# Kernel tuning notes

Measured on AMD Instinct MI355X. Metric: run time of the kernel, lower is better.

The kernel has to match this reference:

```python
import jax, jax.numpy as jnp
import numpy as np

N, L, LEADS = 512, 640, 3
COND_DIM, NUM_K, DIM_K = 1, 100, 5
FLAT = 256 * 79  # 20224, from conv stack trace


def _leaky(x):
    return jnp.where(x >= 0, x, 0.2 * x)


def _sn(w, u):
    # PyTorch spectral_norm: one power iteration (u, v detached), sigma = u^T W v
    wm = w.reshape(w.shape[0], -1)
    v = wm.T @ u
    v = v / (jnp.linalg.norm(v) + 1e-12)
    u2 = wm @ v
    u2 = u2 / (jnp.linalg.norm(u2) + 1e-12)
    u2 = jax.lax.stop_gradient(u2)
    v = jax.lax.stop_gradient(v)
    sigma = u2 @ (wm @ v)
    return w / sigma


def _conv1d(x, w, b, stride, pad):
    y = jax.lax.conv_general_dilated(
        x, w, window_strides=(stride,), padding=[(pad, pad)],
        dimension_numbers=('NCH', 'OIH', 'NCH'))
    return y + b[None, :, None]


def setup_inputs() -> dict:
    key = jax.random.key(0)
    ks = jax.random.split(key, 16)
    g = lambda k, shp, s: (jax.random.normal(k, shp, dtype=jnp.float32) * s)
    inp = {
        'ecg': jax.random.normal(ks[0], (N, L, LEADS), dtype=jnp.float32),
        'condition': jax.random.randint(ks[1], (N, 1), 0, 4),
        'w1': g(ks[2], (64, LEADS, 5), 0.2), 'b1': jnp.zeros((64,), jnp.float32),
        'u1': jax.random.normal(ks[3], (64,), dtype=jnp.float32),
        'w2': g(ks[4], (128, 64, 7), 0.05), 'b2': jnp.zeros((128,), jnp.float32),
        'u2': jax.random.normal(ks[5], (128,), dtype=jnp.float32),
        'w3': g(ks[6], (256, 128, 9), 0.03), 'b3': jnp.zeros((256,), jnp.float32),
        'u3': jax.random.normal(ks[7], (256,), dtype=jnp.float32),
        'emb': g(ks[8], (4, COND_DIM), 1.0),
        'cond_w': g(ks[9], (50, COND_DIM), 0.5), 'cond_b': jnp.zeros((50,), jnp.float32),
        'mb_w': g(ks[10], (FLAT, NUM_K * DIM_K), 0.01),
        'fc_w': g(ks[11], (1, FLAT + NUM_K + 50), 0.01), 'fc_b': jnp.zeros((1,), jnp.float32),
    }
    return inp


def reference(ecg, condition, w1, b1, u1, w2, b2, u2, w3, b3, u3,
              emb, cond_w, cond_b, mb_w, fc_w, fc_b):
    # condition embedding -> Linear(cond_dim, 50)
    cemb = emb[condition[:, 0]]                       # [N, cond_dim]
    cond = cemb @ cond_w.T + cond_b                   # [N, 50]

    x = ecg.transpose(0, 2, 1)                        # [N, 3, 640]
    x = _leaky(_conv1d(x, _sn(w1, u1), b1, 2, 4))     # [N, 64, 322]
    x = _leaky(_conv1d(x, _sn(w2, u2), b2, 2, 3))     # [N, 128, 161]
    x = _leaky(_conv1d(x, _sn(w3, u3), b3, 2, 2))     # [N, 256, 79]
    flat = x.reshape(x.shape[0], -1)                  # [N, 20224]

    # minibatch discrimination
    act = (flat @ mb_w).reshape(-1, NUM_K, DIM_K)     # [N, K, D]
    l1 = jnp.abs(act[:, None] - act[None, :]).sum(-1)  # [N, N, K]
    feats = jnp.exp(-l1).sum(axis=1)                  # [N, K]

    out = jnp.concatenate([flat, feats, cond], axis=1)
    return out @ fc_w.T + fc_b                        # [N, 1]
```

## Files before the change

kernel.cpp:

```cpp
#include <hip/hip_runtime.h>
#include <math.h>

#define NB 512
#define LIN 640
#define NLEADS 3
#define L1O 322
#define L2O 161
#define L3O 79
#define C1N 64
#define C2N 128
#define C3N 256
#define FLATSZ 20224
#define NUMK 100
#define DIMK 5
#define SPLITK 8

typedef __attribute__((ext_vector_type(8))) short short8;
typedef __attribute__((ext_vector_type(4))) float f32x4;

__device__ __forceinline__ unsigned short f2bf(float x){
  unsigned u = __builtin_bit_cast(unsigned, x);
  unsigned r = u + 0x7FFFu + ((u >> 16) & 1u);
  return (unsigned short)(r >> 16);
}
__device__ __forceinline__ float bf2f(unsigned short x){
  unsigned u = ((unsigned)x) << 16;
  return __builtin_bit_cast(float, u);
}

__device__ __forceinline__ float block_reduce_sum(float val, float* red){
#pragma unroll
  for(int off=32; off>0; off>>=1) val += __shfl_down(val, off, 64);
  int lane = threadIdx.x & 63;
  int wv = threadIdx.x >> 6;
  if(lane==0) red[wv] = val;
  __syncthreads();
  int nw = blockDim.x >> 6;
  float r = red[0];
  for(int i=1;i<nw;i++) r += red[i];
  __syncthreads();
  return r;
}

__global__ __launch_bounds__(256)
void sn_pass1(const float* __restrict__ w1, const float* __restrict__ u1,
              const float* __restrict__ w2, const float* __restrict__ u2,
              const float* __restrict__ w3, const float* __restrict__ u3,
              float* __restrict__ v_all, float* __restrict__ ss){
  __shared__ float red[4];
  int b = blockIdx.x, tid = threadIdx.x;
  const float* w; const float* u; int O, C, off, c, widx;
  if(b==0){ w=w1; u=u1; O=64;  C=15;   off=0;   c=tid;            widx=0; }
  else if(b<3){ w=w2; u=u2; O=128; C=448; off=16;  c=(b-1)*256+tid; widx=1; }
  else { w=w3; u=u3; O=256; C=1152; off=464; c=(b-3)*256+tid;      widx=2; }
  float vv = 0.f;
  if(c < C){
    for(int o=0;o<O;o+=4){
      vv += w[(o+0)*C+c]*u[o+0] + w[(o+1)*C+c]*u[o+1]
          + w[(o+2)*C+c]*u[o+2] + w[(o+3)*C+c]*u[o+3];
    }
    v_all[off + c] = vv;
  }
  float ps = (c < C) ? vv*vv : 0.f;
  float tot = block_reduce_sum(ps, red);
  if(tid==0) atomicAdd(&ss[widx], tot);
}

__global__ __launch_bounds__(256)
void sn_pass2(const float* __restrict__ w1, const float* __restrict__ w2,
              const float* __restrict__ w3, const float* __restrict__ v_all,
              float* __restrict__ Sun){
  int b = blockIdx.x, tid = threadIdx.x;
  int lane = tid & 63, wv = tid >> 6;
  const float* w; int C, off, o, widx;
  if(b < 16){ w=w1; C=15;   off=0;   o=b*4+wv;      widx=0; }
  else if(b < 48){ w=w2; C=448; off=16;  o=(b-16)*4+wv; widx=1; }
  else { w=w3; C=1152; off=464; o=(b-48)*4+wv;          widx=2; }
  float t = 0.f;
  for(int c=lane; c<C; c+=64) t += w[o*C+c]*v_all[off+c];
#pragma unroll
  for(int s=32; s>0; s>>=1) t += __shfl_down(t, s, 64);
  if(lane==0) atomicAdd(&Sun[widx], t*t);
}

__global__ void wprep_kernel(const float* __restrict__ w1, const float* __restrict__ w2,
                             const float* __restrict__ w3, const float* __restrict__ ss,
                             const float* __restrict__ Sun,
                             unsigned short* __restrict__ w1p, unsigned short* __restrict__ w2p,
                             unsigned short* __restrict__ w3p){
  float sc[3];
#pragma unroll
  for(int i=0;i<3;i++){
    float inv = 1.f/(sqrtf(ss[i])+1e-12f);
    float S = Sun[i]*inv*inv;
    sc[i] = (sqrtf(S)+1e-12f)/S;
  }
  int idx = blockIdx.x*256 + threadIdx.x;
  if(idx < C1N*32){
    int o = idx >> 5, kk = idx & 31;
    w1p[idx] = (kk < 15) ? f2bf(w1[o*15+kk]*sc[0]) : 0;
  }
  if(idx < C2N*448){
    int o = idx / 448, k2 = idx - o*448;
    int r = k2 >> 6, i = k2 & 63;
    w2p[idx] = f2bf(w2[o*448 + i*7 + r]*sc[1]);
  }
  if(idx < C3N*1152){
    int o = idx / 1152, k2 = idx - o*1152;
    int r = k2 >> 7, i = k2 & 127;
    w3p[idx] = f2bf(w3[o*1152 + i*9 + r]*sc[2]);
  }
}

__global__ __launch_bounds__(256, 2)
void conv123_mfma(const float* __restrict__ ecg, const unsigned short* __restrict__ w1p,
                  const float* __restrict__ b1, const unsigned short* __restrict__ w2p,
                  const float* __restrict__ b2, const unsigned short* __restrict__ w3p,
                  const float* __restrict__ b3, unsigned short* __restrict__ flatbf){
  __shared__ unsigned short y2buf[22712];
  __shared__ unsigned short slabs[13600];
  __shared__ unsigned short B1s[3328];
  int n = blockIdx.x, tid = threadIdx.x;
  int lane = tid & 63, w = tid >> 6;

  if(tid < 136){
    y2buf[tid] = 0;
    y2buf[82*136 + tid] = 0;
    y2buf[83*136 + tid] = 0;
    y2buf[11424 + tid] = 0;
    y2buf[11424 + 81*136 + tid] = 0;
    y2buf[11424 + 82*136 + tid] = 0;
  }

  const float* eb = ecg + (size_t)n*LIN*NLEADS;
  f32x4 zero4 = {0.f,0.f,0.f,0.f};

  for(int tile=0; tile<2; tile++){
    int c0    = tile ? 189 : 0;
    int tbase = tile ? 96  : 0;
    int suboff= tile ? -94 : 2;

    __syncthreads();
    {
      uint4 z = {0u,0u,0u,0u};
      uint4* zd = (uint4*)slabs;
#pragma unroll
      for(int q=0;q<7;q++){
        int f = q*256 + tid;
        if(f < 1700) zd[f] = z;
      }
    }
    if(tid < 208){
      int t1 = c0 + tid;
      int p0 = 2*t1 - 4;
      unsigned short row16[16];
      row16[15] = 0;
      if(p0 >= 0 && p0 <= 635){
        const float* f = eb + p0*NLEADS;
#pragma unroll
        for(int rp=0; rp<5; rp++)
#pragma unroll
          for(int i=0;i<3;i++)
            row16[i*5+rp] = f2bf(f[3*rp+i]);
      } else {
#pragma unroll
        for(int rp=0; rp<5; rp++){
          int p = p0 + rp;
          bool ok = (unsigned)p < (unsigned)LIN;
#pragma unroll
          for(int i=0;i<3;i++)
            row16[i*5+rp] = ok ? f2bf(eb[p*NLEADS+i]) : (unsigned short)0;
        }
      }
      unsigned* dst = (unsigned*)(B1s + tid*16);
#pragma unroll
      for(int q=0;q<8;q++)
        dst[q] = (unsigned)row16[2*q] | ((unsigned)row16[2*q+1] << 16);
    }
    __syncthreads();

    {
      short8 a1 = *(const short8*)(w1p + ((w*16 + (lane&15))<<5) + (lane>>4)*8);
      int cfrag = lane >> 4;
#pragma unroll
      for(int half=0; half<2; half++){
        int nt0 = half*7, ntc = half ? 6 : 7;
        f32x4 c1[7];
        for(int j=0;j<ntc;j++){
          int tp = (nt0+j)*16 + (lane&15);
          short8 b = {0,0,0,0,0,0,0,0};
          if(cfrag < 2) b = *(const short8*)(B1s + tp*16 + cfrag*8);
          c1[j] = __builtin_amdgcn_mfma_f32_16x16x32_bf16(a1, b, zero4, 0, 0, 0);
        }
#pragma unroll
        for(int reg=0;reg<4;reg++){
          int o = w*16 + (lane>>4)*4 + reg;
          float bias = b1[o];
          for(int j=0;j<ntc;j++){
            int tp = (nt0+j)*16 + (lane&15);
            int t1 = c0 + tp;
            int sub = (t1>>1) + suboff;
            if(t1 < L1O && sub < 100){
              float v = c1[j][reg] + bias;
              v = v>=0.f ? v : 0.2f*v;
              slabs[((t1&1)?6800:0) + sub*68 + o] = f2bf(v);
            }
          }
        }
      }
    }
    __syncthreads();

    f32x4 acc[2][6];
#pragma unroll
    for(int i=0;i<2;i++)
#pragma unroll
      for(int j=0;j<6;j++) acc[i][j] = zero4;

    const unsigned short* w2base = w2p + ((size_t)(w*2*16 + (lane&15)))*448 + (lane>>4)*8;
    short8 a_cur[2];
    a_cur[0] = *(const short8*)(w2base);
    a_cur[1] = *(const short8*)(w2base + 16*448);

    for(int ck=0; ck<14; ck++){
      short8 a_nxt[2];
      if(ck < 13){
        a_nxt[0] = *(const short8*)(w2base + (ck+1)*32);
        a_nxt[1] = *(const short8*)(w2base + 16*448 + (ck+1)*32);
      }
      int r = ck >> 1, i0 = (ck & 1)*32;
      int p = (r+1) & 1;
      int m = ((r-3) - p) >> 1;
      int base = (p?6800:0) + (m+2 + (lane&15))*68 + i0 + (lane>>4)*8;
      short8 b[6];
#pragma unroll
      for(int nt=0;nt<6;nt++)
        b[nt] = *(const short8*)(slabs + base + nt*16*68);
      __builtin_amdgcn_s_setprio(1);
#pragma unroll
      for(int mm=0;mm<2;mm++)
#pragma unroll
        for(int nt=0;nt<6;nt++)
          acc[mm][nt] = __builtin_amdgcn_mfma_f32_16x16x32_bf16(a_cur[mm], b[nt], acc[mm][nt], 0, 0, 0);
      __builtin_amdgcn_s_setprio(0);
      if(ck < 13){ a_cur[0] = a_nxt[0]; a_cur[1] = a_nxt[1]; }
    }

#pragma unroll
    for(int mm=0;mm<2;mm++){
#pragma unroll
      for(int reg=0;reg<4;reg++){
        int o = (w*2+mm)*16 + (lane>>4)*4 + reg;
        float bias = b2[o];
#pragma unroll
        for(int nt=0;nt<6;nt++){
          int tl = nt*16 + (lane&15);
          int t = tbase + tl;
          if(t < L2O){
            float v = acc[mm][nt][reg] + bias;
            v = v>=0.f ? v : 0.2f*v;
            y2buf[((t&1)?11424:0) + ((t>>1)+1)*136 + o] = f2bf(v);
          }
        }
      }
    }
  }
  __syncthreads();

  f32x4 acc3[4][5];
#pragma unroll
  for(int i=0;i<4;i++)
#pragma unroll
    for(int j=0;j<5;j++) acc3[i][j] = zero4;

  const unsigned short* wbase = w3p + ((size_t)(w*64) + (lane&15))*1152 + (lane>>4)*8;
  short8 abuf[3][4];
#pragma unroll
  for(int d=0; d<2; d++)
#pragma unroll
    for(int mm=0;mm<4;mm++)
      abuf[d][mm] = *(const short8*)(wbase + mm*16*1152 + d*32);

#pragma unroll
  for(int ck=0; ck<36; ck++){
    const int cur = ck % 3;
    const int nxt = (ck+2) % 3;
    if(ck+2 < 36){
      int kc = (ck+2)*32;
#pragma unroll
      for(int mm=0;mm<4;mm++)
        abuf[nxt][mm] = *(const short8*)(wbase + mm*16*1152 + kc);
    }
    int r = ck >> 2, i0 = (ck & 3) * 32;
    int cbase = ((r & 1) ? 11424 : 0) + (r >> 1)*136 + i0 + (lane>>4)*8;
    short8 b[5];
#pragma unroll
    for(int nt=0;nt<5;nt++){
      int t = nt*16 + (lane&15);
      b[nt] = *(const short8*)(y2buf + cbase + t*136);
    }
    __builtin_amdgcn_s_setprio(1);
#pragma unroll
    for(int mm=0;mm<4;mm++)
#pragma unroll
      for(int nt=0;nt<5;nt++)
        acc3[mm][nt] = __builtin_amdgcn_mfma_f32_16x16x32_bf16(abuf[cur][mm], b[nt], acc3[mm][nt], 0, 0, 0);
    __builtin_amdgcn_s_setprio(0);
  }
#pragma unroll
  for(int mm=0;mm<4;mm++){
#pragma unroll
    for(int reg=0;reg<4;reg++){
      int o = w*64 + mm*16 + (lane>>4)*4 + reg;
      float bias = b3[o];
#pragma unroll
      for(int nt=0;nt<5;nt++){
        int t = nt*16 + (lane&15);
        if(t < L3O){
          float v = acc3[mm][nt][reg] + bias;
          v = v>=0.f ? v : 0.2f*v;
          flatbf[(size_t)n*FLATSZ + o*L3O + t] = f2bf(v);
        }
      }
    }
  }
}

__global__ __launch_bounds__(256)
void mbw_transpose(const float* __restrict__ mbw, unsigned short* __restrict__ mbwT){
  __shared__ unsigned short tile[32][36];
  int k0 = blockIdx.x*32, n0 = blockIdx.y*32, tid = threadIdx.x;
  int r = tid >> 3, c4 = (tid & 7) * 4;
  int nbase = n0 + c4;
  if(nbase + 3 < 500){
    float4 v = *(const float4*)(mbw + (size_t)(k0+r)*500 + nbase);
    tile[r][c4+0] = f2bf(v.x);
    tile[r][c4+1] = f2bf(v.y);
    tile[r][c4+2] = f2bf(v.z);
    tile[r][c4+3] = f2bf(v.w);
  } else {
#pragma unroll
    for(int j=0;j<4;j++){
      int nn = nbase + j;
      float v = (nn < 500) ? mbw[(size_t)(k0+r)*500 + nn] : 0.f;
      tile[r][c4+j] = f2bf(v);
    }
  }
  __syncthreads();
  int nl = tid >> 3, kq = (tid & 7) * 4;
  unsigned short t0 = tile[kq+0][nl], t1 = tile[kq+1][nl];
  unsigned short t2 = tile[kq+2][nl], t3 = tile[kq+3][nl];
  uint2 p;
  p.x = (unsigned)t0 | ((unsigned)t1 << 16);
  p.y = (unsigned)t2 | ((unsigned)t3 << 16);
  *(uint2*)(mbwT + (size_t)(n0+nl)*FLATSZ + k0 + kq) = p;
}

__global__ __launch_bounds__(256)
void mb_gemm_mfma(const unsigned short* __restrict__ flatbf, const unsigned short* __restrict__ mbwT,
                  float* __restrict__ part){
  __shared__ unsigned short As[64*32];
  __shared__ unsigned short Bs[64*32];
  int tid = threadIdx.x;
  int lane = tid & 63, w = tid >> 6;
  int m0 = blockIdx.x*64, n0 = blockIdx.y*64, bz = blockIdx.z;
  int t_count = 79;
  int k0 = bz*79*32;
  f32x4 zero = {0.f,0.f,0.f,0.f};
  f32x4 acc[4];
#pragma unroll
  for(int i=0;i<4;i++) acc[i] = zero;
  int arow = tid >> 2, acol = (tid & 3) * 8;
  for(int t=0; t<t_count; t++, k0+=32){
    __syncthreads();
    ((uint4*)As)[tid] = *(const uint4*)(flatbf + (size_t)(m0+arow)*FLATSZ + k0 + acol);
    ((uint4*)Bs)[tid] = *(const uint4*)(mbwT  + (size_t)(n0+arow)*FLATSZ + k0 + acol);
    __syncthreads();
    short8 a = *(const short8*)(As + (w*16 + (lane&15))*32 + (lane>>4)*8);
#pragma unroll
    for(int nt=0;nt<4;nt++){
      short8 b = *(const short8*)(Bs + (nt*16 + (lane&15))*32 + (lane>>4)*8);
      acc[nt] = __builtin_amdgcn_mfma_f32_16x16x32_bf16(a, b, acc[nt], 0, 0, 0);
    }
  }
  float* po = part + (size_t)bz*NB*500;
#pragma unroll
  for(int nt=0;nt<4;nt++){
#pragma unroll
    for(int reg=0;reg<4;reg++){
      int m = m0 + w*16 + (lane>>4)*4 + reg;
      int c = n0 + nt*16 + (lane&15);
      if(c < 500) po[(size_t)m*500 + c] = acc[nt][reg];
    }
  }
}

__global__ void mb_reduce_kernel(const float* __restrict__ part, float* __restrict__ actT){
  int idx = blockIdx.x*256 + threadIdx.x;
  float s = 0.f;
#pragma unroll
  for(int z=0;z<SPLITK;z++) s += part[(size_t)z*NB*500 + idx];
  int n = idx/500, c = idx - n*500;
  actT[(size_t)c*NB + n] = s;
}

__global__ __launch_bounds__(256)
void feats_kernel(const float* __restrict__ actT, float* __restrict__ feats){
  __shared__ float ash[4][50];
  __shared__ float pred[4][4];
  int i0 = blockIdx.x*4, k0 = blockIdx.y*10;
  int tid = threadIdx.x, lane = tid & 63, wv = tid >> 6;
  if(tid < 200){
    int ii = tid/50, c = tid - ii*50;
    ash[ii][c] = actT[(size_t)(k0*5+c)*NB + i0 + ii];
  }
  __syncthreads();
  const float LOG2E = 1.4426950408889634f;
  int j1 = tid, j2 = tid + 256;
  for(int kk=0; kk<10; kk++){
    const float* r0 = actT + (size_t)(k0+kk)*5*NB;
    float xa0=r0[j1], xa1=r0[NB+j1], xa2=r0[2*NB+j1], xa3=r0[3*NB+j1], xa4=r0[4*NB+j1];
    float xb0=r0[j2], xb1=r0[NB+j2], xb2=r0[2*NB+j2], xb3=r0[3*NB+j2], xb4=r0[4*NB+j2];
    float f[4];
#pragma unroll
    for(int ii=0; ii<4; ii++){
      float a0=ash[ii][kk*5+0], a1=ash[ii][kk*5+1], a2=ash[ii][kk*5+2],
            a3=ash[ii][kk*5+3], a4=ash[ii][kk*5+4];
      float la = fabsf(xa0-a0)+fabsf(xa1-a1)+fabsf(xa2-a2)+fabsf(xa3-a3)+fabsf(xa4-a4);
      float lb = fabsf(xb0-a0)+fabsf(xb1-a1)+fabsf(xb2-a2)+fabsf(xb3-a3)+fabsf(xb4-a4);
      f[ii] = exp2f(-LOG2E*la) + exp2f(-LOG2E*lb);
    }
#pragma unroll
    for(int ii=0; ii<4; ii++){
      float v = f[ii];
#pragma unroll
      for(int s=32; s>0; s>>=1) v += __shfl_down(v, s, 64);
      if(lane==0) pred[wv][ii] = v;
    }
    __syncthreads();
    if(tid < 4){
      float v = pred[0][tid] + pred[1][tid] + pred[2][tid] + pred[3][tid];
      feats[(size_t)(i0+tid)*NUMK + k0 + kk] = v;
    }
    __syncthreads();
  }
}

__global__ void final_kernel(const unsigned short* __restrict__ flatbf, const float* __restrict__ feats,
                             const int* __restrict__ condition, const float* __restrict__ emb,
                             const float* __restrict__ cond_w, const float* __restrict__ cond_b,
                             const float* __restrict__ fc_w, const float* __restrict__ fc_b,
                             float* __restrict__ out){
  __shared__ float red[4];
  int n = blockIdx.x, tid = threadIdx.x;
  float s = 0.f;
  const unsigned short* fr = flatbf + (size_t)n*FLATSZ;
  for(int q=tid; q<FLATSZ/8; q+=256){
    uint4 u = *(const uint4*)(fr + q*8);
    float4 wa = *(const float4*)(fc_w + q*8);
    float4 wb = *(const float4*)(fc_w + q*8 + 4);
    s += bf2f((unsigned short)(u.x & 0xffff))*wa.x + bf2f((unsigned short)(u.x >> 16))*wa.y
       + bf2f((unsigned short)(u.y & 0xffff))*wa.z + bf2f((unsigned short)(u.y >> 16))*wa.w
       + bf2f((unsigned short)(u.z & 0xffff))*wb.x + bf2f((unsigned short)(u.z >> 16))*wb.y
       + bf2f((unsigned short)(u.w & 0xffff))*wb.z + bf2f((unsigned short)(u.w >> 16))*wb.w;
  }
  for(int k=tid;k<NUMK;k+=256) s += feats[n*NUMK+k]*fc_w[FLATSZ+k];
  float ce = emb[condition[n]];
  for(int j=tid;j<50;j+=256) s += (ce*cond_w[j]+cond_b[j])*fc_w[FLATSZ+NUMK+j];
  s = block_reduce_sum(s, red);
  if(tid==0) out[n] = s + fc_b[0];
}

extern "C" void kernel_launch(void* const* d_in, const int* in_sizes, int n_in,
                              void* d_out, int out_size, void* d_ws, size_t ws_size,
                              hipStream_t stream) {
  const float* ecg   = (const float*)d_in[0];
  const int*   cond  = (const int*)  d_in[1];
  const float* w1    = (const float*)d_in[2];
  const float* b1    = (const float*)d_in[3];
  const float* u1    = (const float*)d_in[4];
  const float* w2    = (const float*)d_in[5];
  const float* b2    = (const float*)d_in[6];
  const float* u2    = (const float*)d_in[7];
  const float* w3    = (const float*)d_in[8];
  const float* b3    = (const float*)d_in[9];
  const float* u3    = (const float*)d_in[10];
  const float* emb   = (const float*)d_in[11];
  const float* condw = (const float*)d_in[12];
  const float* condb = (const float*)d_in[13];
  const float* mbw   = (const float*)d_in[14];
  const float* fcw   = (const float*)d_in[15];
  const float* fcb   = (const float*)d_in[16];

  float* ws = (float*)d_ws;
  float* ssbuf = ws + 16;
  float* Sunbuf= ws + 24;
  float* v_all = ws + 32;
  unsigned short* w1p  = (unsigned short*)(ws + 1648);
  unsigned short* w2p  = (unsigned short*)(ws + 2672);
  unsigned short* w3p  = (unsigned short*)(ws + 31344);
  unsigned short* mbwT = (unsigned short*)(ws + 178800);
  float* part  = ws + 5454448;
  float* actT  = ws + 9550448;
  float* feats = ws + 9806448;
  unsigned short* flatbf = (unsigned short*)(ws + 9857648);

  hipMemsetAsync((char*)d_ws + 64, 0, 64, stream);
  sn_pass1<<<8, 256, 0, stream>>>(w1,u1,w2,u2,w3,u3, v_all, ssbuf);
  sn_pass2<<<112, 256, 0, stream>>>(w1,w2,w3, v_all, Sunbuf);
  wprep_kernel<<<1152, 256, 0, stream>>>(w1, w2, w3, ssbuf, Sunbuf, w1p, w2p, w3p);
  conv123_mfma<<<NB, 256, 0, stream>>>(ecg, w1p, b1, w2p, b2, w3p, b3, flatbf);
  mbw_transpose<<<dim3(632,16), 256, 0, stream>>>(mbw, mbwT);
  mb_gemm_mfma<<<dim3(8,8,SPLITK), 256, 0, stream>>>(flatbf, mbwT, part);
  mb_reduce_kernel<<<1000, 256, 0, stream>>>(part, actT);
  feats_kernel<<<dim3(128,10), 256, 0, stream>>>(actT, feats);
  final_kernel<<<NB, 256, 0, stream>>>(flatbf, feats, cond, emb, condw, condb, fcw, fcb, (float*)d_out);
}
```

Baseline: 309.0 us.

## Load MFMA operands directly from global and double split-K in minibatch GEMM

```diff
diff --git a/kernel.cpp b/kernel.cpp
--- a/kernel.cpp
+++ b/kernel.cpp
@@ -13,7 +13,7 @@
 #define FLATSZ 20224
 #define NUMK 100
 #define DIMK 5
-#define SPLITK 8
+#define SPLITK 16
 
 typedef __attribute__((ext_vector_type(8))) short short8;
 typedef __attribute__((ext_vector_type(4))) float f32x4;
@@ -356,32 +356,34 @@
   *(uint2*)(mbwT + (size_t)(n0+nl)*FLATSZ + k0 + kq) = p;
 }
 
-__global__ __launch_bounds__(256)
+__global__ __launch_bounds__(256, 4)
 void mb_gemm_mfma(const unsigned short* __restrict__ flatbf, const unsigned short* __restrict__ mbwT,
                   float* __restrict__ part){
-  __shared__ unsigned short As[64*32];
-  __shared__ unsigned short Bs[64*32];
   int tid = threadIdx.x;
   int lane = tid & 63, w = tid >> 6;
   int m0 = blockIdx.x*64, n0 = blockIdx.y*64, bz = blockIdx.z;
-  int t_count = 79;
-  int k0 = bz*79*32;
+  int t_start = bz*39 + (bz<8 ? bz : 8);
+  int t_count = 39 + (bz<8 ? 1 : 0);
   f32x4 zero = {0.f,0.f,0.f,0.f};
   f32x4 acc[4];
 #pragma unroll
   for(int i=0;i<4;i++) acc[i] = zero;
-  int arow = tid >> 2, acol = (tid & 3) * 8;
-  for(int t=0; t<t_count; t++, k0+=32){
-    __syncthreads();
-    ((uint4*)As)[tid] = *(const uint4*)(flatbf + (size_t)(m0+arow)*FLATSZ + k0 + acol);
-    ((uint4*)Bs)[tid] = *(const uint4*)(mbwT  + (size_t)(n0+arow)*FLATSZ + k0 + acol);
-    __syncthreads();
-    short8 a = *(const short8*)(As + (w*16 + (lane&15))*32 + (lane>>4)*8);
-#pragma unroll
-    for(int nt=0;nt<4;nt++){
-      short8 b = *(const short8*)(Bs + (nt*16 + (lane&15))*32 + (lane>>4)*8);
-      acc[nt] = __builtin_amdgcn_mfma_f32_16x16x32_bf16(a, b, acc[nt], 0, 0, 0);
-    }
+
+  const unsigned short* abase = flatbf + (size_t)(m0 + w*16 + (lane&15))*FLATSZ + (lane>>4)*8 + t_start*32;
+  const unsigned short* bbase = mbwT  + (size_t)(n0 + (lane&15))*FLATSZ + (lane>>4)*8 + t_start*32;
+
+#pragma unroll 2
+  for(int t=0; t<t_count; t++){
+    int kk = t*32;
+    short8 a  = *(const short8*)(abase + kk);
+    short8 b0 = *(const short8*)(bbase + kk);
+    short8 b1 = *(const short8*)(bbase + (size_t)16*FLATSZ + kk);
+    short8 b2 = *(const short8*)(bbase + (size_t)32*FLATSZ + kk);
+    short8 b3 = *(const short8*)(bbase + (size_t)48*FLATSZ + kk);
+    acc[0] = __builtin_amdgcn_mfma_f32_16x16x32_bf16(a, b0, acc[0], 0, 0, 0);
+    acc[1] = __builtin_amdgcn_mfma_f32_16x16x32_bf16(a, b1, acc[1], 0, 0, 0);
+    acc[2] = __builtin_amdgcn_mfma_f32_16x16x32_bf16(a, b2, acc[2], 0, 0, 0);
+    acc[3] = __builtin_amdgcn_mfma_f32_16x16x32_bf16(a, b3, acc[3], 0, 0, 0);
   }
   float* po = part + (size_t)bz*NB*500;
 #pragma unroll
```

Measured after the change: 352.0 us. +13.9%, slower.

## Double-buffer and swizzle minibatch GEMM LDS tiles with register prefetch, split-K 16

Applied to the files above, without the earlier changes.

```diff
diff --git a/kernel.cpp b/kernel.cpp
--- a/kernel.cpp
+++ b/kernel.cpp
@@ -13,7 +13,7 @@
 #define FLATSZ 20224
 #define NUMK 100
 #define DIMK 5
-#define SPLITK 8
+#define SPLITK 16
 
 typedef __attribute__((ext_vector_type(8))) short short8;
 typedef __attribute__((ext_vector_type(4))) float f32x4;
@@ -356,32 +356,82 @@
   *(uint2*)(mbwT + (size_t)(n0+nl)*FLATSZ + k0 + kq) = p;
 }
 
-__global__ __launch_bounds__(256)
+__global__ __launch_bounds__(256, 4)
 void mb_gemm_mfma(const unsigned short* __restrict__ flatbf, const unsigned short* __restrict__ mbwT,
                   float* __restrict__ part){
-  __shared__ unsigned short As[64*32];
-  __shared__ unsigned short Bs[64*32];
+  __shared__ unsigned short As[2][4096];
+  __shared__ unsigned short Bs[2][4096];
   int tid = threadIdx.x;
   int lane = tid & 63, w = tid >> 6;
   int m0 = blockIdx.x*64, n0 = blockIdx.y*64, bz = blockIdx.z;
-  int t_count = 79;
-  int k0 = bz*79*32;
+  int s_start = bz*19 + (bz < 12 ? bz : 12);
+  int s_count = 19 + (bz < 12 ? 1 : 0);
+
+  int r0 = tid >> 3,        c80 = tid & 7;
+  int r1 = 32 + (tid >> 3), c81 = tid & 7;
+  const unsigned short* aptr0 = flatbf + (size_t)(m0+r0)*FLATSZ + c80*8;
+  const unsigned short* aptr1 = flatbf + (size_t)(m0+r1)*FLATSZ + c81*8;
+  const unsigned short* bptr0 = mbwT  + (size_t)(n0+r0)*FLATSZ + c80*8;
+  const unsigned short* bptr1 = mbwT  + (size_t)(n0+r1)*FLATSZ + c81*8;
+  int d0 = r0*64 + ((c80 ^ (r0 & 7)) * 8);
+  int d1 = r1*64 + ((c81 ^ (r1 & 7)) * 8);
+
   f32x4 zero = {0.f,0.f,0.f,0.f};
   f32x4 acc[4];
 #pragma unroll
   for(int i=0;i<4;i++) acc[i] = zero;
-  int arow = tid >> 2, acol = (tid & 3) * 8;
-  for(int t=0; t<t_count; t++, k0+=32){
+
+  int arow = w*16 + (lane&15);
+  int af0 = arow*64 + ((((lane>>4)  ) ^ (arow & 7)) * 8);
+  int af1 = arow*64 + (((4+(lane>>4)) ^ (arow & 7)) * 8);
+  int bf0[4], bf1[4];
+#pragma unroll
+  for(int nt=0;nt<4;nt++){
+    int br = nt*16 + (lane&15);
+    bf0[nt] = br*64 + ((((lane>>4)  ) ^ (br & 7)) * 8);
+    bf1[nt] = br*64 + (((4+(lane>>4)) ^ (br & 7)) * 8);
+  }
+
+  size_t koff = (size_t)s_start * 64;
+  uint4 ra0 = *(const uint4*)(aptr0 + koff);
+  uint4 ra1 = *(const uint4*)(aptr1 + koff);
+  uint4 rb0 = *(const uint4*)(bptr0 + koff);
+  uint4 rb1 = *(const uint4*)(bptr1 + koff);
+
+  for(int s=0; s<s_count; s++){
+    int cur = s & 1;
+    *(uint4*)(As[cur] + d0) = ra0;
+    *(uint4*)(As[cur] + d1) = ra1;
+    *(uint4*)(Bs[cur] + d0) = rb0;
+    *(uint4*)(Bs[cur] + d1) = rb1;
+    koff += 64;
+    if(s+1 < s_count){
+      ra0 = *(const uint4*)(aptr0 + koff);
+      ra1 = *(const uint4*)(aptr1 + koff);
+      rb0 = *(const uint4*)(bptr0 + koff);
+      rb1 = *(const uint4*)(bptr1 + koff);
+    }
     __syncthreads();
-    ((uint4*)As)[tid] = *(const uint4*)(flatbf + (size_t)(m0+arow)*FLATSZ + k0 + acol);
-    ((uint4*)Bs)[tid] = *(const uint4*)(mbwT  + (size_t)(n0+arow)*FLATSZ + k0 + acol);
-    __syncthreads();
-    short8 a = *(const short8*)(As + (w*16 + (lane&15))*32 + (lane>>4)*8);
-#pragma unroll
-    for(int nt=0;nt<4;nt++){
-      short8 b = *(const short8*)(Bs + (nt*16 + (lane&15))*32 + (lane>>4)*8);
-      acc[nt] = __builtin_amdgcn_mfma_f32_16x16x32_bf16(a, b, acc[nt], 0, 0, 0);
-    }
+    short8 a0 = *(const short8*)(As[cur] + af0);
+    short8 a1 = *(const short8*)(As[cur] + af1);
+    short8 b0h0 = *(const short8*)(Bs[cur] + bf0[0]);
+    short8 b1h0 = *(const short8*)(Bs[cur] + bf0[1]);
+    short8 b2h0 = *(const short8*)(Bs[cur] + bf0[2]);
+    short8 b3h0 = *(const short8*)(Bs[cur] + bf0[3]);
+    short8 b0h1 = *(const short8*)(Bs[cur] + bf1[0]);
+    short8 b1h1 = *(const short8*)(Bs[cur] + bf1[1]);
+    short8 b2h1 = *(const short8*)(Bs[cur] + bf1[2]);
+    short8 b3h1 = *(const short8*)(Bs[cur] + bf1[3]);
+    __builtin_amdgcn_s_setprio(1);
+    acc[0] = __builtin_amdgcn_mfma_f32_16x16x32_bf16(a0, b0h0, acc[0], 0, 0, 0);
+    acc[1] = __builtin_amdgcn_mfma_f32_16x16x32_bf16(a0, b1h0, acc[1], 0, 0, 0);
+    acc[2] = __builtin_amdgcn_mfma_f32_16x16x32_bf16(a0, b2h0, acc[2], 0, 0, 0);
+    acc[3] = __builtin_amdgcn_mfma_f32_16x16x32_bf16(a0, b3h0, acc[3], 0, 0, 0);
+    acc[0] = __builtin_amdgcn_mfma_f32_16x16x32_bf16(a1, b0h1, acc[0], 0, 0, 0);
+    acc[1] = __builtin_amdgcn_mfma_f32_16x16x32_bf16(a1, b1h1, acc[1], 0, 0, 0);
+    acc[2] = __builtin_amdgcn_mfma_f32_16x16x32_bf16(a1, b2h1, acc[2], 0, 0, 0);
+    acc[3] = __builtin_amdgcn_mfma_f32_16x16x32_bf16(a1, b3h1, acc[3], 0, 0, 0);
+    __builtin_amdgcn_s_setprio(0);
   }
   float* po = part + (size_t)bz*NB*500;
 #pragma unroll
```

After: 292.4 us. 5.4% less time.
